# Optimization experiments

Measured on AMD Instinct MI355X. Metric: run time of the kernel, lower is better.

Reference implementation:

```python
import jax, jax.numpy as jnp
import numpy as np

BATCH = 16384
N_FEAT = 2048
SWAP_PROB = 0.1


def setup_inputs() -> dict:
    key = jax.random.key(0)
    k_x, k_mask, k_perm = jax.random.split(key, 3)
    x = jax.random.normal(k_x, (BATCH, N_FEAT), dtype=jnp.float32)
    # swap_mask[i, j] = True with prob swap_prob (matches torch.rand(...) < swap_prob)
    swap_mask = jax.random.uniform(k_mask, (BATCH, N_FEAT)) < SWAP_PROB
    # per-row random permutation (matches torch.randperm per batch row),
    # vectorized as argsort of iid uniforms
    perm = jnp.argsort(jax.random.uniform(k_perm, (BATCH, N_FEAT)), axis=1).astype(jnp.int32)
    return {"x": x, "swap_mask": swap_mask, "perm": perm}


def reference(x, swap_mask, perm):
    # x[i, swap_mask[i]] = x[i, perm[i][swap_mask[i]]]  (vectorized over rows)
    swapped = jnp.take_along_axis(x, perm, axis=1)  # [B, F]
    return jnp.where(swap_mask, swapped, x)
```

## Files before the change

### kernel.cpp

```cpp
#include <hip/hip_runtime.h>

#define NFEAT 2048
#define BATCH 16384

__global__ __launch_bounds__(256) void swap_corrupt_kernel(
    const float* __restrict__ x,
    const int*   __restrict__ mask,
    const int*   __restrict__ perm,
    float*       __restrict__ out)
{
    __shared__ float row[NFEAT];

    const int r = blockIdx.x;
    const int t = threadIdx.x;
    const size_t base = (size_t)r * NFEAT;

    const float4* __restrict__ x4 = (const float4*)(x + base);
    float4 a = x4[t];
    float4 b = x4[t + 256];
    ((float4*)row)[t]       = a;
    ((float4*)row)[t + 256] = b;
    __syncthreads();

    const int4* __restrict__ m4 = (const int4*)(mask + base);
    const int4* __restrict__ p4 = (const int4*)(perm + base);
    float4* __restrict__ o4 = (float4*)(out + base);

    {
        int4 m = m4[t];
        int4 p = p4[t];
        float4 o;
        o.x = m.x ? row[p.x] : a.x;
        o.y = m.y ? row[p.y] : a.y;
        o.z = m.z ? row[p.z] : a.z;
        o.w = m.w ? row[p.w] : a.w;
        o4[t] = o;
    }
    {
        int4 m = m4[t + 256];
        int4 p = p4[t + 256];
        float4 o;
        o.x = m.x ? row[p.x] : b.x;
        o.y = m.y ? row[p.y] : b.y;
        o.z = m.z ? row[p.z] : b.z;
        o.w = m.w ? row[p.w] : b.w;
        o4[t + 256] = o;
    }
}

extern "C" void kernel_launch(void* const* d_in, const int* in_sizes, int n_in,
                              void* d_out, int out_size, void* d_ws, size_t ws_size,
                              hipStream_t stream) {
    const float* x    = (const float*)d_in[0];
    const int*   mask = (const int*)d_in[1];
    const int*   perm = (const int*)d_in[2];
    float*       out  = (float*)d_out;

    swap_corrupt_kernel<<<dim3(BATCH), dim3(256), 0, stream>>>(x, mask, perm, out);
}
```

Measured before the change: 381.2 us.

## Assign one row per wavefront and stage x into LDS via direct global_load_lds

Each 256-thread block now handles four rows, one per 64-lane wavefront, so the block-wide __syncthreads is no longer needed. The x row is copied straight from global memory into LDS with the global_load_lds builtin while mask and perm are loaded into registers, and a single vmcnt wait covers all of them. Every output element is then read from LDS, using either the permuted index or its own position. The aim is more memory traffic in flight per wave and no register round-trip for x. In exchange it needs 32KB of LDS per block and more registers, and it relies on an inline-asm wait to order the LDS writes.

```diff
diff --git a/kernel.cpp b/kernel.cpp
--- a/kernel.cpp
+++ b/kernel.cpp
@@ -2,6 +2,7 @@
 
 #define NFEAT 2048
 #define BATCH 16384
+#define WPB   4
 
 __global__ __launch_bounds__(256) void swap_corrupt_kernel(
     const float* __restrict__ x,
@@ -9,42 +10,46 @@
     const int*   __restrict__ perm,
     float*       __restrict__ out)
 {
-    __shared__ float row[NFEAT];
+    __shared__ float rows[WPB][NFEAT];
 
-    const int r = blockIdx.x;
-    const int t = threadIdx.x;
+    const int t    = threadIdx.x;
+    const int w    = t >> 6;
+    const int lane = t & 63;
+    const int r    = blockIdx.x * WPB + w;
     const size_t base = (size_t)r * NFEAT;
 
-    const float4* __restrict__ x4 = (const float4*)(x + base);
-    float4 a = x4[t];
-    float4 b = x4[t + 256];
-    ((float4*)row)[t]       = a;
-    ((float4*)row)[t + 256] = b;
-    __syncthreads();
+    auto* lrow = (__attribute__((address_space(3))) float*)(&rows[w][0]);
+    const auto* gx = (const __attribute__((address_space(1))) float*)(x + base);
+#pragma unroll
+    for (int c = 0; c < 8; ++c) {
+        __builtin_amdgcn_global_load_lds(
+            (const __attribute__((address_space(1))) void*)(gx + c * 256 + lane * 4),
+            (__attribute__((address_space(3))) void*)(lrow + c * 256),
+            16, 0, 0);
+    }
 
     const int4* __restrict__ m4 = (const int4*)(mask + base);
     const int4* __restrict__ p4 = (const int4*)(perm + base);
+    int4 m[8], p[8];
+#pragma unroll
+    for (int c = 0; c < 8; ++c) {
+        m[c] = m4[c * 64 + lane];
+        p[c] = p4[c * 64 + lane];
+    }
+
+    asm volatile("s_waitcnt vmcnt(0)" ::: "memory");
+
+    const float* row = &rows[w][0];
     float4* __restrict__ o4 = (float4*)(out + base);
-
-    {
-        int4 m = m4[t];
-        int4 p = p4[t];
+#pragma unroll
+    for (int c = 0; c < 8; ++c) {
+        const int e0 = c * 256 + lane * 4;
         float4 o;
-        o.x = m.x ? row[p.x] : a.x;
-        o.y = m.y ? row[p.y] : a.y;
-        o.z = m.z ? row[p.z] : a.z;
-        o.w = m.w ? row[p.w] : a.w;
-        o4[t] = o;
-    }
-    {
-        int4 m = m4[t + 256];
-        int4 p = p4[t + 256];
-        float4 o;
-        o.x = m.x ? row[p.x] : b.x;
-        o.y = m.y ? row[p.y] : b.y;
-        o.z = m.z ? row[p.z] : b.z;
-        o.w = m.w ? row[p.w] : b.w;
-        o4[t + 256] = o;
+        o.x = row[m[c].x ? p[c].x : e0    ];
+        o.y = row[m[c].y ? p[c].y : e0 + 1];
+        o.z = row[m[c].z ? p[c].z : e0 + 2];
+        o.w = row[m[c].w ? p[c].w : e0 + 3];
+        o4[c * 64 + lane] = o;
     }
 }
 
@@ -56,5 +61,5 @@
     const int*   perm = (const int*)d_in[2];
     float*       out  = (float*)d_out;
 
-    swap_corrupt_kernel<<<dim3(BATCH), dim3(256), 0, stream>>>(x, mask, perm, out);
+    swap_corrupt_kernel<<<dim3(BATCH / WPB), dim3(256), 0, stream>>>(x, mask, perm, out);
 }
```

Result: no change. 388.1 us (+1.8%).
